# Kernel optimization log

Hardware: AMD Instinct MI355X
Metric: run time of the kernel (lower is better)

The kernel has to match this reference:

```python
import jax, jax.numpy as jnp
import numpy as np

NTYPE = 4
ALPHA = 0.2  # LeakyReLU negative slope
N_NODES = 65536
N_FEAT = 64
N_HEADS = 4
BATCH = 131072


def setup_inputs() -> dict:
    key = jax.random.key(0)
    k1, k2, k3 = jax.random.split(key, 3)
    total = BATCH * NTYPE  # 524288 = 8 * N_NODES -> guarantees full node coverage
    ids = jnp.tile(jnp.arange(N_NODES, dtype=jnp.int64 if jax.config.jax_enable_x64 else jnp.int32), total // N_NODES)
    batch = jax.random.permutation(k1, ids).reshape(BATCH, NTYPE)
    batch_features = jax.random.normal(k2, (N_NODES, N_FEAT), dtype=jnp.float32)
    att_weights = jax.random.normal(k3, (N_HEADS, NTYPE - 1), dtype=jnp.float32) * 0.1
    return {"batch": batch, "batch_features": batch_features, "att_weights": att_weights}


def reference(batch, batch_features, att_weights):
    ntype = NTYPE
    B = batch.shape[0]
    N, F = batch_features.shape
    # filters = ~eye(ntype): for row i, keep all columns except i
    cols = np.stack([[j for j in range(ntype) if j != i] for i in range(ntype)])  # [ntype, ntype-1]
    # neighbor indices per (filter i, batch row b): batch[b, cols[i]]
    neigh = jnp.transpose(batch[:, cols], (1, 0, 2)).reshape(ntype * B, ntype - 1)  # [ntype*B, ntype-1]
    feat = batch_features[neigh]  # gather: [ntype*B, ntype-1, F]
    # att_feat = att_weights @ feat (broadcast matmul): [ntype*B, a, F]
    att_feat = jnp.einsum('ak,rkf->raf', att_weights, feat)
    # target node of each feat row: batch.T.flatten()
    batch_nodes = batch.T.reshape(-1)  # [ntype*B]
    # max-pool rows per node (nodes = 0..N-1 by construction): [N, a, F]
    agg = jax.ops.segment_max(att_feat, batch_nodes, num_segments=N)
    agg = jnp.transpose(agg, (1, 0, 2))  # [a, N, F]
    out = batch_features[None, :, :] + agg  # broadcast add: [a, N, F]
    out = jnp.transpose(out, (1, 0, 2))  # [N, a, F]
    out = jax.nn.leaky_relu(out, negative_slope=ALPHA)
    return out.reshape(N, -1)  # concat=True -> [N, a*F]
```

## Files before the change

kernel.cpp:

```cpp
#include <hip/hip_runtime.h>
#include <hip/hip_fp16.h>

#define N_NODES 65536
#define N_FEAT  64
#define N_HEADS 4
#define BATCHSZ 131072
#define NTYPE   4
#define ALPHA   0.2f
#define SRC_PER_NODE 8

typedef float f32x4 __attribute__((ext_vector_type(4)));

__global__ __launch_bounds__(256) void to_half(const float* __restrict__ feat,
                                               __half* __restrict__ feat_h) {
    int i = (blockIdx.x * 256 + threadIdx.x) * 8;
    float4 a = *(const float4*)(feat + i);
    float4 b = *(const float4*)(feat + i + 4);
    __half2 h0 = __floats2half2_rn(a.x, a.y);
    __half2 h1 = __floats2half2_rn(a.z, a.w);
    __half2 h2 = __floats2half2_rn(b.x, b.y);
    __half2 h3 = __floats2half2_rn(b.z, b.w);
    uint4 o;
    o.x = __builtin_bit_cast(unsigned int, h0);
    o.y = __builtin_bit_cast(unsigned int, h1);
    o.z = __builtin_bit_cast(unsigned int, h2);
    o.w = __builtin_bit_cast(unsigned int, h3);
    *(uint4*)(feat_h + i) = o;
}

__global__ __launch_bounds__(256) void build_index(const int* __restrict__ batch,
                                                   int* __restrict__ cnt,
                                                   int2* __restrict__ idx2) {
    int b = blockIdx.x * blockDim.x + threadIdx.x;
    int4 br = ((const int4*)batch)[b];
    int p0 = atomicAdd(&cnt[br.x], 1);
    int p1 = atomicAdd(&cnt[br.y], 1);
    int p2 = atomicAdd(&cnt[br.z], 1);
    int p3 = atomicAdd(&cnt[br.w], 1);
    if (p0 < SRC_PER_NODE) idx2[br.x * SRC_PER_NODE + p0] = make_int2(br.y | (br.z << 16), br.w);
    if (p1 < SRC_PER_NODE) idx2[br.y * SRC_PER_NODE + p1] = make_int2(br.x | (br.z << 16), br.w);
    if (p2 < SRC_PER_NODE) idx2[br.z * SRC_PER_NODE + p2] = make_int2(br.x | (br.y << 16), br.w);
    if (p3 < SRC_PER_NODE) idx2[br.w * SRC_PER_NODE + p3] = make_int2(br.x | (br.y << 16), br.z);
}


__device__ __forceinline__ float4 f4max(float4 a, float4 b) {
    return make_float4(fmaxf(a.x, b.x), fmaxf(a.y, b.y), fmaxf(a.z, b.z), fmaxf(a.w, b.w));
}
__device__ __forceinline__ float4 f4shflx(float4 v, int m) {
    return make_float4(__shfl_xor(v.x, m), __shfl_xor(v.y, m), __shfl_xor(v.z, m), __shfl_xor(v.w, m));
}
__device__ __forceinline__ float4 f4mix(float w0, float w1, float w2, float4 a, float4 b, float4 c) {
    return make_float4(fmaf(w0, a.x, fmaf(w1, b.x, w2 * c.x)),
                       fmaf(w0, a.y, fmaf(w1, b.y, w2 * c.y)),
                       fmaf(w0, a.z, fmaf(w1, b.z, w2 * c.z)),
                       fmaf(w0, a.w, fmaf(w1, b.w, w2 * c.w)));
}
__device__ __forceinline__ float4 loadh4(const __half* p) {
    uint2 r = *(const uint2*)p;
    float2 f01 = __half22float2(__builtin_bit_cast(__half2, r.x));
    float2 f23 = __half22float2(__builtin_bit_cast(__half2, r.y));
    return make_float4(f01.x, f01.y, f23.x, f23.y);
}

__global__ __launch_bounds__(256) void gat_agg(const float* __restrict__ feat,
                                               const __half* __restrict__ feat_h,
                                               const float* __restrict__ att,
                                               const int2* __restrict__ idx2,
                                               float* __restrict__ out) {
    const int wave = threadIdx.x >> 6;
    const int lane = threadIdx.x & 63;
    const int q    = lane >> 4;
    const int fl   = lane & 15;
    const int t = blockIdx.x * 4 + wave;

    float w[N_HEADS][3];
    #pragma unroll
    for (int a = 0; a < N_HEADS; ++a)
        #pragma unroll
        for (int k = 0; k < 3; ++k)
            w[a][k] = att[a * 3 + k];

    int4 s = ((const int4*)(idx2 + t * SRC_PER_NODE))[q];
    int a0 = s.x & 0xffff, a1 = ((unsigned)s.x) >> 16, a2 = s.y & 0xffff;
    int b0 = s.z & 0xffff, b1 = ((unsigned)s.z) >> 16, b2 = s.w & 0xffff;

    float4 m0 = make_float4(-INFINITY, -INFINITY, -INFINITY, -INFINITY);
    float4 m1 = m0, m2 = m0, m3 = m0;

    #define DO_SRC(N0, N1, N2) {                                                 \
        float4 f0 = loadh4(feat_h + (N0) * N_FEAT + 4 * fl);                     \
        float4 f1 = loadh4(feat_h + (N1) * N_FEAT + 4 * fl);                     \
        float4 f2 = loadh4(feat_h + (N2) * N_FEAT + 4 * fl);                     \
        m0 = f4max(m0, f4mix(w[0][0], w[0][1], w[0][2], f0, f1, f2));            \
        m1 = f4max(m1, f4mix(w[1][0], w[1][1], w[1][2], f0, f1, f2));            \
        m2 = f4max(m2, f4mix(w[2][0], w[2][1], w[2][2], f0, f1, f2));            \
        m3 = f4max(m3, f4mix(w[3][0], w[3][1], w[3][2], f0, f1, f2));            \
    }

    DO_SRC(a0, a1, a2);
    DO_SRC(b0, b1, b2);
    #undef DO_SRC

    m0 = f4max(m0, f4shflx(m0, 16));  m0 = f4max(m0, f4shflx(m0, 32));
    m1 = f4max(m1, f4shflx(m1, 16));  m1 = f4max(m1, f4shflx(m1, 32));
    m2 = f4max(m2, f4shflx(m2, 16));  m2 = f4max(m2, f4shflx(m2, 32));
    m3 = f4max(m3, f4shflx(m3, 16));  m3 = f4max(m3, f4shflx(m3, 32));

    float4 sel = (q < 2) ? ((q == 0) ? m0 : m1) : ((q == 2) ? m2 : m3);
    float4 ft = *(const float4*)(feat + t * N_FEAT + 4 * fl);
    float4 o = make_float4(ft.x + sel.x, ft.y + sel.y, ft.z + sel.z, ft.w + sel.w);
    o.x = fmaxf(o.x, ALPHA * o.x);
    o.y = fmaxf(o.y, ALPHA * o.y);
    o.z = fmaxf(o.z, ALPHA * o.z);
    o.w = fmaxf(o.w, ALPHA * o.w);
    f32x4 ov = {o.x, o.y, o.z, o.w};
    __builtin_nontemporal_store(ov, (f32x4*)(out + t * (N_HEADS * N_FEAT) + 4 * lane));
}

extern "C" void kernel_launch(void* const* d_in, const int* in_sizes, int n_in,
                              void* d_out, int out_size, void* d_ws, size_t ws_size,
                              hipStream_t stream) {
    const int*   batch = (const int*)d_in[0];
    const float* feat  = (const float*)d_in[1];
    const float* att   = (const float*)d_in[2];
    float* out = (float*)d_out;

    char* ws = (char*)d_ws;
    int*    cnt    = (int*)ws;
    int2*   idx2   = (int2*)(ws + N_NODES * sizeof(int));
    __half* feat_h = (__half*)(ws + N_NODES * sizeof(int)
                                  + N_NODES * SRC_PER_NODE * sizeof(int2));

    hipMemsetAsync(cnt, 0, N_NODES * sizeof(int), stream);
    to_half<<<(N_NODES * N_FEAT) / (256 * 8), 256, 0, stream>>>(feat, feat_h);
    build_index<<<BATCHSZ / 256, 256, 0, stream>>>(batch, cnt, idx2);
    gat_agg<<<N_NODES / 4, 256, 0, stream>>>(feat, feat_h, att, idx2, out);
}
```

Before: 140.4 us.

## Slice fp16 feature table into per-16-feature planes and compute in half2

```diff
diff --git a/kernel.cpp b/kernel.cpp
--- a/kernel.cpp
+++ b/kernel.cpp
@@ -5,27 +5,35 @@
 #define N_FEAT  64
 #define N_HEADS 4
 #define BATCHSZ 131072
-#define NTYPE   4
 #define ALPHA   0.2f
 #define SRC_PER_NODE 8
+#define NSLICE   4
+#define SLICE_F  16
 
-typedef float f32x4 __attribute__((ext_vector_type(4)));
+typedef float f32x2 __attribute__((ext_vector_type(2)));
 
-__global__ __launch_bounds__(256) void to_half(const float* __restrict__ feat,
-                                               __half* __restrict__ feat_h) {
+__device__ __forceinline__ __half2 h2max(__half2 a, __half2 b) {
+    __half2 r;
+    r.x = __hmax(a.x, b.x);
+    r.y = __hmax(a.y, b.y);
+    return r;
+}
+
+__global__ __launch_bounds__(256) void to_half_sliced(const float* __restrict__ feat,
+                                                      __half* __restrict__ feat_s) {
     int i = (blockIdx.x * 256 + threadIdx.x) * 8;
+    int n   = i >> 6;
+    int f0  = i & 63;
+    int s   = f0 >> 4;
+    int off = f0 & 15;
     float4 a = *(const float4*)(feat + i);
     float4 b = *(const float4*)(feat + i + 4);
-    __half2 h0 = __floats2half2_rn(a.x, a.y);
-    __half2 h1 = __floats2half2_rn(a.z, a.w);
-    __half2 h2 = __floats2half2_rn(b.x, b.y);
-    __half2 h3 = __floats2half2_rn(b.z, b.w);
     uint4 o;
-    o.x = __builtin_bit_cast(unsigned int, h0);
-    o.y = __builtin_bit_cast(unsigned int, h1);
-    o.z = __builtin_bit_cast(unsigned int, h2);
-    o.w = __builtin_bit_cast(unsigned int, h3);
-    *(uint4*)(feat_h + i) = o;
+    o.x = __builtin_bit_cast(unsigned int, __floats2half2_rn(a.x, a.y));
+    o.y = __builtin_bit_cast(unsigned int, __floats2half2_rn(a.z, a.w));
+    o.z = __builtin_bit_cast(unsigned int, __floats2half2_rn(b.x, b.y));
+    o.w = __builtin_bit_cast(unsigned int, __floats2half2_rn(b.z, b.w));
+    *(uint4*)(feat_s + (s * N_NODES + n) * SLICE_F + off) = o;
 }
 
 __global__ __launch_bounds__(256) void build_index(const int* __restrict__ batch,
@@ -43,79 +51,60 @@
     if (p3 < SRC_PER_NODE) idx2[br.w * SRC_PER_NODE + p3] = make_int2(br.x | (br.y << 16), br.z);
 }
 
+__global__ __launch_bounds__(256) void gat_agg_sliced(const __half* __restrict__ feat_s,
+                                                      const float* __restrict__ att,
+                                                      const int2* __restrict__ idx2,
+                                                      float* __restrict__ out) {
+    const int wave  = threadIdx.x >> 6;
+    const int lane  = threadIdx.x & 63;
+    const int src   = lane >> 3;
+    const int fp    = lane & 7;
+    const int slice = blockIdx.x & 3;
+    const int t     = (blockIdx.x >> 2) * 4 + wave;
 
-__device__ __forceinline__ float4 f4max(float4 a, float4 b) {
-    return make_float4(fmaxf(a.x, b.x), fmaxf(a.y, b.y), fmaxf(a.z, b.z), fmaxf(a.w, b.w));
-}
-__device__ __forceinline__ float4 f4shflx(float4 v, int m) {
-    return make_float4(__shfl_xor(v.x, m), __shfl_xor(v.y, m), __shfl_xor(v.z, m), __shfl_xor(v.w, m));
-}
-__device__ __forceinline__ float4 f4mix(float w0, float w1, float w2, float4 a, float4 b, float4 c) {
-    return make_float4(fmaf(w0, a.x, fmaf(w1, b.x, w2 * c.x)),
-                       fmaf(w0, a.y, fmaf(w1, b.y, w2 * c.y)),
-                       fmaf(w0, a.z, fmaf(w1, b.z, w2 * c.z)),
-                       fmaf(w0, a.w, fmaf(w1, b.w, w2 * c.w)));
-}
-__device__ __forceinline__ float4 loadh4(const __half* p) {
-    uint2 r = *(const uint2*)p;
-    float2 f01 = __half22float2(__builtin_bit_cast(__half2, r.x));
-    float2 f23 = __half22float2(__builtin_bit_cast(__half2, r.y));
-    return make_float4(f01.x, f01.y, f23.x, f23.y);
-}
-
-__global__ __launch_bounds__(256) void gat_agg(const float* __restrict__ feat,
-                                               const __half* __restrict__ feat_h,
-                                               const float* __restrict__ att,
-                                               const int2* __restrict__ idx2,
-                                               float* __restrict__ out) {
-    const int wave = threadIdx.x >> 6;
-    const int lane = threadIdx.x & 63;
-    const int q    = lane >> 4;
-    const int fl   = lane & 15;
-    const int t = blockIdx.x * 4 + wave;
-
-    float w[N_HEADS][3];
+    __half2 w2[N_HEADS][3];
     #pragma unroll
     for (int a = 0; a < N_HEADS; ++a)
         #pragma unroll
         for (int k = 0; k < 3; ++k)
-            w[a][k] = att[a * 3 + k];
+            w2[a][k] = __float2half2_rn(att[a * 3 + k]);
 
-    int4 s = ((const int4*)(idx2 + t * SRC_PER_NODE))[q];
-    int a0 = s.x & 0xffff, a1 = ((unsigned)s.x) >> 16, a2 = s.y & 0xffff;
-    int b0 = s.z & 0xffff, b1 = ((unsigned)s.z) >> 16, b2 = s.w & 0xffff;
+    int2 nb = idx2[t * SRC_PER_NODE + src];
+    int n0 = nb.x & 0xffff;
+    int n1 = ((unsigned)nb.x) >> 16;
+    int n2 = nb.y & 0xffff;
 
-    float4 m0 = make_float4(-INFINITY, -INFINITY, -INFINITY, -INFINITY);
-    float4 m1 = m0, m2 = m0, m3 = m0;
+    const __half* plane = feat_s + slice * (N_NODES * SLICE_F);
 
-    #define DO_SRC(N0, N1, N2) {                                                 \
-        float4 f0 = loadh4(feat_h + (N0) * N_FEAT + 4 * fl);                     \
-        float4 f1 = loadh4(feat_h + (N1) * N_FEAT + 4 * fl);                     \
-        float4 f2 = loadh4(feat_h + (N2) * N_FEAT + 4 * fl);                     \
-        m0 = f4max(m0, f4mix(w[0][0], w[0][1], w[0][2], f0, f1, f2));            \
-        m1 = f4max(m1, f4mix(w[1][0], w[1][1], w[1][2], f0, f1, f2));            \
-        m2 = f4max(m2, f4mix(w[2][0], w[2][1], w[2][2], f0, f1, f2));            \
-        m3 = f4max(m3, f4mix(w[3][0], w[3][1], w[3][2], f0, f1, f2));            \
+    __half2 f0 = __builtin_bit_cast(__half2, *(const unsigned int*)(plane + n0 * SLICE_F + 2 * fp));
+    __half2 f1 = __builtin_bit_cast(__half2, *(const unsigned int*)(plane + n1 * SLICE_F + 2 * fp));
+    __half2 f2 = __builtin_bit_cast(__half2, *(const unsigned int*)(plane + n2 * SLICE_F + 2 * fp));
+
+    __half2 v0 = __hfma2(w2[0][0], f0, __hfma2(w2[0][1], f1, __hmul2(w2[0][2], f2)));
+    __half2 v1 = __hfma2(w2[1][0], f0, __hfma2(w2[1][1], f1, __hmul2(w2[1][2], f2)));
+    __half2 v2 = __hfma2(w2[2][0], f0, __hfma2(w2[2][1], f1, __hmul2(w2[2][2], f2)));
+    __half2 v3 = __hfma2(w2[3][0], f0, __hfma2(w2[3][1], f1, __hmul2(w2[3][2], f2)));
+
+    #define BFLY(V) {                                                              \
+        V = h2max(V, __builtin_bit_cast(__half2, __shfl_xor(__builtin_bit_cast(int, V),  8))); \
+        V = h2max(V, __builtin_bit_cast(__half2, __shfl_xor(__builtin_bit_cast(int, V), 16))); \
+        V = h2max(V, __builtin_bit_cast(__half2, __shfl_xor(__builtin_bit_cast(int, V), 32))); \
     }
+    BFLY(v0); BFLY(v1); BFLY(v2); BFLY(v3);
+    #undef BFLY
 
-    DO_SRC(a0, a1, a2);
-    DO_SRC(b0, b1, b2);
-    #undef DO_SRC
-
-    m0 = f4max(m0, f4shflx(m0, 16));  m0 = f4max(m0, f4shflx(m0, 32));
-    m1 = f4max(m1, f4shflx(m1, 16));  m1 = f4max(m1, f4shflx(m1, 32));
-    m2 = f4max(m2, f4shflx(m2, 16));  m2 = f4max(m2, f4shflx(m2, 32));
-    m3 = f4max(m3, f4shflx(m3, 16));  m3 = f4max(m3, f4shflx(m3, 32));
-
-    float4 sel = (q < 2) ? ((q == 0) ? m0 : m1) : ((q == 2) ? m2 : m3);
-    float4 ft = *(const float4*)(feat + t * N_FEAT + 4 * fl);
-    float4 o = make_float4(ft.x + sel.x, ft.y + sel.y, ft.z + sel.z, ft.w + sel.w);
-    o.x = fmaxf(o.x, ALPHA * o.x);
-    o.y = fmaxf(o.y, ALPHA * o.y);
-    o.z = fmaxf(o.z, ALPHA * o.z);
-    o.w = fmaxf(o.w, ALPHA * o.w);
-    f32x4 ov = {o.x, o.y, o.z, o.w};
-    __builtin_nontemporal_store(ov, (f32x4*)(out + t * (N_HEADS * N_FEAT) + 4 * lane));
+    if (lane < 32) {
+        int a = lane >> 3;
+        __half2 mv = (a < 2) ? ((a == 0) ? v0 : v1) : ((a == 2) ? v2 : v3);
+        float2 mf = __half22float2(mv);
+        float2 fs = __half22float2(__builtin_bit_cast(__half2,
+                        *(const unsigned int*)(plane + t * SLICE_F + 2 * fp)));
+        float ox = fs.x + mf.x; ox = fmaxf(ox, ALPHA * ox);
+        float oy = fs.y + mf.y; oy = fmaxf(oy, ALPHA * oy);
+        f32x2 ov = {ox, oy};
+        __builtin_nontemporal_store(ov,
+            (f32x2*)(out + t * (N_HEADS * N_FEAT) + a * N_FEAT + slice * SLICE_F + 2 * fp));
+    }
 }
 
 extern "C" void kernel_launch(void* const* d_in, const int* in_sizes, int n_in,
@@ -129,11 +118,11 @@
     char* ws = (char*)d_ws;
     int*    cnt    = (int*)ws;
     int2*   idx2   = (int2*)(ws + N_NODES * sizeof(int));
-    __half* feat_h = (__half*)(ws + N_NODES * sizeof(int)
+    __half* feat_s = (__half*)(ws + N_NODES * sizeof(int)
                                   + N_NODES * SRC_PER_NODE * sizeof(int2));
 
     hipMemsetAsync(cnt, 0, N_NODES * sizeof(int), stream);
-    to_half<<<(N_NODES * N_FEAT) / (256 * 8), 256, 0, stream>>>(feat, feat_h);
+    to_half_sliced<<<(N_NODES * N_FEAT) / (256 * 8), 256, 0, stream>>>(feat, feat_s);
     build_index<<<BATCHSZ / 256, 256, 0, stream>>>(batch, cnt, idx2);
-    gat_agg<<<N_NODES / 4, 256, 0, stream>>>(feat, feat_h, att, idx2, out);
+    gat_agg_sliced<<<(N_NODES / 4) * NSLICE, 256, 0, stream>>>(feat_s, att, idx2, out);
 }
```

Result: slower. 239.0 us (+70.3%).
